# Optimization experiments

Measured on AMD Instinct MI355X. Metric: run time of the kernel, lower is better.

Reference implementation:

```python
import jax, jax.numpy as jnp
import numpy as np

QMIN, QMAX = 0.0, 255.0
# activation statistics (min, max) per layer, from init_kwargs['stats']
STATS = {"conv1": (-0.5, 3.0), "conv2": (0.0, 6.0), "fc1": (0.0, 8.0), "fc2": (0.0, 10.0)}


def calc_scale_zp(min_val, max_val):
    scale = (max_val - min_val) / (QMAX - QMIN)
    # original: int(clamped initial zero point) -> truncation
    zp = jnp.trunc(jnp.clip(QMIN - min_val / scale, QMIN, QMAX))
    return scale, zp


def quantize(x, min_val=None, max_val=None):
    if min_val is None:
        min_val, max_val = x.min(), x.max()
    scale, zp = calc_scale_zp(min_val, max_val)
    q = jnp.round(jnp.clip(zp + x / scale, QMIN, QMAX))
    return q, scale, zp


def conv2d(x, w, b):
    y = jax.lax.conv_general_dilated(x, w, (1, 1), "VALID",
                                     dimension_numbers=("NCHW", "OIHW", "NCHW"))
    return y + b[None, :, None, None]


def linear(x, w, b):
    return x @ w.T + b


def max_pool_2x2(x):
    return jax.lax.reduce_window(x, -jnp.inf, jax.lax.max, (1, 1, 2, 2), (1, 1, 2, 2), "VALID")


def quantize_layer(q_x, scale_x, zp_x, W, B, apply_fn, stat):
    # fake-quant weights/bias with their own min/max
    wq, scale_w, zp_w = quantize(W)
    bq, scale_b, zp_b = quantize(B)
    scale_next, zp_next = calc_scale_zp(stat[0], stat[1])
    X = q_x - zp_x
    W_eff = scale_x * scale_w * (wq - zp_w)
    B_eff = scale_b * (bq + zp_b)  # '+ zp_b' is faithful to the source
    y = jax.nn.relu(apply_fn(X, W_eff, B_eff) / scale_next + zp_next)
    # .round().byte() in torch wraps mod 256
    return jnp.mod(jnp.round(y), 256.0), scale_next, zp_next


def setup_inputs() -> dict:
    key = jax.random.key(0)
    ks = jax.random.split(key, 9)
    B = 4096
    return {
        "x": jax.random.normal(ks[0], (B, 1, 28, 28), jnp.float32),
        "conv1_w": jax.random.normal(ks[1], (20, 1, 5, 5), jnp.float32) * 0.1,
        "conv1_b": jax.random.normal(ks[2], (20,), jnp.float32) * 0.1,
        "conv2_w": jax.random.normal(ks[3], (50, 20, 5, 5), jnp.float32) * 0.05,
        "conv2_b": jax.random.normal(ks[4], (50,), jnp.float32) * 0.05,
        "fc1_w": jax.random.normal(ks[5], (500, 800), jnp.float32) * 0.03,
        "fc1_b": jax.random.normal(ks[6], (500,), jnp.float32) * 0.03,
        "fc2_w": jax.random.normal(ks[7], (10, 500), jnp.float32) * 0.05,
        "fc2_b": jax.random.normal(ks[8], (10,), jnp.float32) * 0.05,
    }


def reference(x, conv1_w, conv1_b, conv2_w, conv2_b, fc1_w, fc1_b, fc2_w, fc2_b):
    q, s, zp = quantize(x, STATS["conv1"][0], STATS["conv1"][1])
    q, s, zp = quantize_layer(q, s, zp, conv1_w, conv1_b, conv2d, STATS["conv2"])
    q = max_pool_2x2(q)                       # [B,20,12,12]
    q, s, zp = quantize_layer(q, s, zp, conv2_w, conv2_b, conv2d, STATS["fc1"])
    q = max_pool_2x2(q)                       # [B,50,4,4]
    q = q.reshape(-1, 4 * 4 * 50)             # [B,800]
    q, s, zp = quantize_layer(q, s, zp, fc1_w, fc1_b, linear, STATS["fc2"])
    xf = s * (q - zp)                         # dequantize
    logits = linear(xf, fc2_w, fc2_b)         # [B,10]
    return jax.nn.log_softmax(logits, axis=1)
```

## Files before the change

### kernel.cpp

```cpp
#include <hip/hip_runtime.h>
#include <cmath>

#define TPB 256
typedef float floatx4 __attribute__((ext_vector_type(4)));
typedef __bf16 bf16x8 __attribute__((ext_vector_type(8)));
typedef unsigned short ushort8 __attribute__((ext_vector_type(8)));
typedef unsigned int uint2v __attribute__((ext_vector_type(2)));
typedef unsigned short ushort_t;

#define OFF_PMN 16
#define OFF_PMX 96
#define OFF_B1 520
#define OFF_B2 544
#define OFF_B3 600
#define W1BF_BYTE 6144
#define W2BF_BYTE 8192
#define W3BF_BYTE 131072
#define PART_BYTE 1048576
#define Q2_BYTE  29360128ULL

#define S_X1 (3.5f/255.0f)
#define ZP_X1 36.0f
#define S_N1 (6.0f/255.0f)
#define S_N2 (8.0f/255.0f)
#define S_N3 (10.0f/255.0f)

#define XSTR 40
#define NCG 4

__device__ inline float qclip(float x, float s, float zp){
    return rintf(fminf(fmaxf(zp + x / s, 0.0f), 255.0f));
}
__device__ inline ushort_t bfbits(float v){
    return (ushort_t)(__float_as_uint(v) >> 16);
}

__global__ __launch_bounds__(TPB) void k_minmax(
        const float* c1w, const float* c1b, const float* c2w, const float* c2b,
        const float* f1w, const float* f1b, float* pmn, float* pmx){
    __shared__ float smn[TPB], smx[TPB];
    int bb = blockIdx.x, tid = threadIdx.x;
    const float* src; int n, sub, nsub;
    if      (bb == 0){ src=c1w; n=500;    sub=0;     nsub=1;  }
    else if (bb == 1){ src=c1b; n=20;     sub=0;     nsub=1;  }
    else if (bb <  6){ src=c2w; n=25000;  sub=bb-2;  nsub=4;  }
    else if (bb == 6){ src=c2b; n=50;     sub=0;     nsub=1;  }
    else if (bb < 71){ src=f1w; n=400000; sub=bb-7;  nsub=64; }
    else             { src=f1b; n=500;    sub=0;     nsub=1;  }
    float mn = INFINITY, mx = -INFINITY;
    for (int i = sub*TPB + tid; i < n; i += nsub*TPB){
        float v = src[i]; mn = fminf(mn, v); mx = fmaxf(mx, v);
    }
    smn[tid] = mn; smx[tid] = mx; __syncthreads();
    for (int s = TPB/2; s > 0; s >>= 1){
        if (tid < s){
            smn[tid] = fminf(smn[tid], smn[tid+s]);
            smx[tid] = fmaxf(smx[tid], smx[tid+s]);
        }
        __syncthreads();
    }
    if (tid == 0){ pmn[bb] = smn[0]; pmx[bb] = smx[0]; }
}

#define N_EFF 452157
__global__ __launch_bounds__(TPB) void k_make_eff(
        const float* c1w, const float* c1b, const float* c2w, const float* c2b,
        const float* f1w, const float* f1b, const float* pmn, const float* pmx,
        float* ws, ushort_t* w1bf, ushort_t* w2bf, ushort_t* w3bf){
    __shared__ float sS[6], sZ[6];
    int tid = threadIdx.x;
    int wv = tid >> 6, lane = tid & 63;
    const int starts[6] = {0,1,2,6,7,71};
    const int counts[6] = {1,1,4,1,64,1};
    #pragma unroll
    for (int rep = 0; rep < 2; ++rep){
        int t = wv + rep*4;
        if (t < 6){
            float mn = INFINITY, mx = -INFINITY;
            if (lane < counts[t]){ mn = pmn[starts[t]+lane]; mx = pmx[starts[t]+lane]; }
            #pragma unroll
            for (int off = 32; off > 0; off >>= 1){
                mn = fminf(mn, __shfl_xor(mn, off));
                mx = fmaxf(mx, __shfl_xor(mx, off));
            }
            if (lane == 0){
                float s = (mx - mn) / 255.0f;
                sS[t] = s;
                sZ[t] = truncf(fminf(fmaxf(0.0f - mn / s, 0.0f), 255.0f));
            }
        }
    }
    __syncthreads();

    int i = blockIdx.x * TPB + tid;
    if (i >= N_EFF) return;
    if (i < 1024){
        int n = i >> 5, k = i & 31;
        float v = 0.0f;
        if (n < 20 && k < 25) v = qclip(c1w[n*25 + k], sS[0], sZ[0]) - sZ[0];
        w1bf[i] = bfbits(v);
    } else if (i < 1044){
        int j = i - 1024;
        ws[OFF_B1 + j] = (sS[1] * (qclip(c1b[j], sS[1], sZ[1]) + sZ[1])) / S_N1;
    } else if (i < 42004){
        int j = i - 1044;
        int c = j >> 11, r = j & 2047, co = r >> 5, k = r & 31;
        int q = k >> 3, jj = k & 7;
        int tap, ci; bool valid;
        if (c < 13){ tap = 2*c + (q>>1); ci = (q&1)*8 + jj; valid = (tap < 25); }
        else       { tap = 4*(c-13) + q; ci = 16 + jj;      valid = (tap < 25) && (jj < 4); }
        valid = valid && (co < 50);
        float v = 0.0f;
        if (valid) v = qclip(c2w[(co*20 + ci)*25 + tap], sS[2], sZ[2]) - sZ[2];
        w2bf[j] = bfbits(v);
    } else if (i < 42054){
        int j = i - 42004;
        ws[OFF_B2 + j] = (sS[3] * (qclip(c2b[j], sS[3], sZ[3]) + sZ[3])) / S_N2;
    } else if (i < 451654){
        int j = i - 42054;
        int n = j / 800, k = j - 800*n;
        float v = 0.0f;
        if (n < 500) v = qclip(f1w[n*800 + k], sS[4], sZ[4]) - sZ[4];
        w3bf[j] = bfbits(v);
    } else if (i < 452154){
        int j = i - 451654;
        ws[OFF_B3 + j] = (sS[5] * (qclip(f1b[j], sS[5], sZ[5]) + sZ[5])) / S_N3;
    } else if (i == 452154){
        ws[0] = (S_N1 * sS[2]) / S_N2;
    } else if (i == 452155){
        ws[1] = (S_N2 * sS[4]) / S_N3;
    } else {
        ws[2] = (S_X1 * sS[0]) / S_N1;
    }
}

__global__ __launch_bounds__(TPB, 4) void k_conv12(const float* x, const ushort_t* w1bf,
                                                   const ushort_t* w2bt, const float* ws,
                                                   ushort_t* q2bf, int B){
    __shared__ __align__(16) ushort_t xs[144*XSTR];
    __shared__ __align__(16) ushort_t xim[3136];
    int b = blockIdx.x, tid = threadIdx.x;
    int lane = tid & 63, wv = tid >> 6;
    int ln = lane & 15, quad = lane >> 4;

    for (int i = tid; i < 144; i += TPB){
        *(unsigned int*)(xs + i*XSTR + 20) = 0u;
        *(unsigned int*)(xs + i*XSTR + 22) = 0u;
    }

    const float* xb = x + (size_t)b * 784;
    if (tid < 196){
        floatx4 v = *(const floatx4*)(xb + tid*4);
        unsigned int qp[2];
        #pragma unroll
        for (int h = 0; h < 2; ++h){
            float q0 = rintf(fminf(fmaxf(ZP_X1 + v[2*h]   / S_X1, 0.0f), 255.0f)) - ZP_X1;
            float q1 = rintf(fminf(fmaxf(ZP_X1 + v[2*h+1] / S_X1, 0.0f), 255.0f)) - ZP_X1;
            qp[h] = (unsigned int)bfbits(q0) | ((unsigned int)bfbits(q1) << 16);
        }
        uint2v qq; qq.x = qp[0]; qq.y = qp[1];
        uint2v* dst = (uint2v*)xim;
        dst[tid]       = qq;
        dst[196 + tid] = qq;
        dst[392 + tid] = qq;
        dst[588 + tid] = qq;
    }

    int offj[8];
    #pragma unroll
    for (int j = 0; j < 8; ++j){
        int k = quad*8 + j;
        int kh = k / 5, kw = k - 5*kh;
        offj[j] = (k < 25) ? (kh*28 + kw) : 0;
    }
    const ushort_t* xq = xim + quad*784;

    ushort8 bw0 = *(const ushort8*)(w1bf + ln*32 + quad*8);
    ushort8 bw1 = *(const ushort8*)(w1bf + (16 + ln)*32 + quad*8);
    bf16x8 bf0 = __builtin_bit_cast(bf16x8, bw0);
    bf16x8 bf1 = __builtin_bit_cast(bf16x8, bw1);

    float K1 = ws[2];
    float B1_0 = ws[OFF_B1 + ln];
    float B1_1 = (ln < 4) ? ws[OFF_B1 + 16 + ln] : 0.0f;
    __syncthreads();

    #pragma unroll 3
    for (int i = 0; i < 9; ++i){
        int mt = 9*wv + i;
        int m = mt*16 + ln;
        int p = m >> 2, crn = m & 3;
        int ph_ = p / 12, pw_ = p - 12*ph_;
        int oh = 2*ph_ + (crn >> 1), ow = 2*pw_ + (crn & 1);
        int base = oh*28 + ow;
        ushort8 aw;
        #pragma unroll
        for (int j = 0; j < 8; ++j)
            aw[j] = xq[base + offj[j]];
        bf16x8 af = __builtin_bit_cast(bf16x8, aw);
        floatx4 z = (floatx4){0.f,0.f,0.f,0.f};
        floatx4 a0 = __builtin_amdgcn_mfma_f32_16x16x32_bf16(af, bf0, z, 0, 0, 0);
        floatx4 a1 = __builtin_amdgcn_mfma_f32_16x16x32_bf16(af, bf1, z, 0, 0, 0);

        int pp = mt*4 + quad;
        {
            float y0 = fmaf(a0[0], K1, B1_0), y1 = fmaf(a0[1], K1, B1_0);
            float y2 = fmaf(a0[2], K1, B1_0), y3 = fmaf(a0[3], K1, B1_0);
            float mA = fmaxf(fmaxf(y0, y1), y2);
            float mf = fmaxf(fmaxf(mA, y3), 0.0f);
            if (__ballot(mf >= 255.5f)){
                unsigned int q0 = ((unsigned int)rintf(fmaxf(y0,0.f))) & 255u;
                unsigned int q1 = ((unsigned int)rintf(fmaxf(y1,0.f))) & 255u;
                unsigned int qq2 = ((unsigned int)rintf(fmaxf(y2,0.f))) & 255u;
                unsigned int q3 = ((unsigned int)rintf(fmaxf(y3,0.f))) & 255u;
                unsigned int h0 = q0 > q1 ? q0 : q1;
                unsigned int h1 = qq2 > q3 ? qq2 : q3;
                mf = (float)(h0 > h1 ? h0 : h1);
            } else {
                mf = rintf(mf);
            }
            xs[pp*XSTR + ln] = bfbits(mf);
        }
        if (ln < 4){
            float y0 = fmaf(a1[0], K1, B1_1), y1 = fmaf(a1[1], K1, B1_1);
            float y2 = fmaf(a1[2], K1, B1_1), y3 = fmaf(a1[3], K1, B1_1);
            float mA = fmaxf(fmaxf(y0, y1), y2);
            float mf = fmaxf(fmaxf(mA, y3), 0.0f);
            if (__ballot(mf >= 255.5f)){
                unsigned int q0 = ((unsigned int)rintf(fmaxf(y0,0.f))) & 255u;
                unsigned int q1 = ((unsigned int)rintf(fmaxf(y1,0.f))) & 255u;
                unsigned int qq2 = ((unsigned int)rintf(fmaxf(y2,0.f))) & 255u;
                unsigned int q3 = ((unsigned int)rintf(fmaxf(y3,0.f))) & 255u;
                unsigned int h0 = q0 > q1 ? q0 : q1;
                unsigned int h1 = qq2 > q3 ? qq2 : q3;
                mf = (float)(h0 > h1 ? h0 : h1);
            } else {
                mf = rintf(mf);
            }
            xs[pp*XSTR + 16 + ln] = bfbits(mf);
        }
    }
    __syncthreads();

    int mt0 = (wv & 1) * 2;
    int nt0 = (wv >> 1) * 2;
    int abase[2];
    #pragma unroll
    for (int mi = 0; mi < 2; ++mi)
        abase[mi] = (24*(mt0+mi) + (ln>>3)*12 + (ln&7)) * XSTR;
    int aoff[20];
    #pragma unroll
    for (int c = 0; c < 20; ++c){
        int tap, inner;
        if (c < 13){ tap = 2*c + (quad>>1); inner = (quad&1)*8; }
        else       { tap = 4*(c-13) + quad; inner = 16; }
        int pt = 0;
        if (tap < 25){ int kh = tap/5, kw = tap-5*kh; pt = kh*12 + kw; }
        aoff[c] = pt*XSTR + inner;
    }

    float sc2d = ws[0];
    const ushort_t* bsrc0 = w2bt + (size_t)(nt0*16 + ln)*32 + quad*8;
    const ushort_t* bsrc1 = bsrc0 + 16*32;

    floatx4 acc[2][2];
    #pragma unroll
    for (int mi = 0; mi < 2; ++mi)
        #pragma unroll
        for (int ni = 0; ni < 2; ++ni) acc[mi][ni] = (floatx4){0.f,0.f,0.f,0.f};

    #pragma unroll
    for (int c = 0; c < 20; ++c){
        ushort8 b0w = *(const ushort8*)(bsrc0 + c*2048);
        ushort8 b1w = *(const ushort8*)(bsrc1 + c*2048);
        ushort8 a0w = *(const ushort8*)(xs + abase[0] + aoff[c]);
        ushort8 a1w = *(const ushort8*)(xs + abase[1] + aoff[c]);
        bf16x8 a0 = __builtin_bit_cast(bf16x8, a0w);
        bf16x8 a1 = __builtin_bit_cast(bf16x8, a1w);
        bf16x8 b0 = __builtin_bit_cast(bf16x8, b0w);
        bf16x8 b1 = __builtin_bit_cast(bf16x8, b1w);
        acc[0][0] = __builtin_amdgcn_mfma_f32_16x16x32_bf16(a0, b0, acc[0][0], 0, 0, 0);
        acc[0][1] = __builtin_amdgcn_mfma_f32_16x16x32_bf16(a0, b1, acc[0][1], 0, 0, 0);
        acc[1][0] = __builtin_amdgcn_mfma_f32_16x16x32_bf16(a1, b0, acc[1][0], 0, 0, 0);
        acc[1][1] = __builtin_amdgcn_mfma_f32_16x16x32_bf16(a1, b1, acc[1][1], 0, 0, 0);
    }

    #pragma unroll
    for (int ni = 0; ni < 2; ++ni){
        int co = (nt0 + ni)*16 + ln;
        float bias2d = (co < 50) ? ws[OFF_B2 + co] : 0.0f;
        #pragma unroll
        for (int mi = 0; mi < 2; ++mi){
            int mt = mt0 + mi;
            float y0 = fmaf(acc[mi][ni][0], sc2d, bias2d);
            float y1 = fmaf(acc[mi][ni][1], sc2d, bias2d);
            float y2 = fmaf(acc[mi][ni][2], sc2d, bias2d);
            float y3 = fmaf(acc[mi][ni][3], sc2d, bias2d);
            float f0 = fmaxf(fmaxf(y0, y1), 0.0f);
            float f1 = fmaxf(fmaxf(y2, y3), 0.0f);
            float g0 = __shfl_xor(f0, 32);
            float g1 = __shfl_xor(f1, 32);
            float v0f = fmaxf(f0, g0), v1f = fmaxf(f1, g1);
            if (__ballot(fmaxf(v0f, v1f) >= 255.5f)){
                unsigned int q0 = ((unsigned int)rintf(fmaxf(y0,0.f))) & 255u;
                unsigned int q1 = ((unsigned int)rintf(fmaxf(y1,0.f))) & 255u;
                unsigned int qq2 = ((unsigned int)rintf(fmaxf(y2,0.f))) & 255u;
                unsigned int q3 = ((unsigned int)rintf(fmaxf(y3,0.f))) & 255u;
                unsigned int h0 = q0 > q1 ? q0 : q1;
                unsigned int h1 = qq2 > q3 ? qq2 : q3;
                unsigned int p0 = (unsigned int)__shfl_xor((int)h0, 32);
                unsigned int p1 = (unsigned int)__shfl_xor((int)h1, 32);
                v0f = (float)(h0 > p0 ? h0 : p0);
                v1f = (float)(h1 > p1 ? h1 : p1);
            } else {
                v0f = rintf(v0f); v1f = rintf(v1f);
            }
            if (quad < 2 && co < 50){
                size_t base = (size_t)b*800 + co*16 + mt*4 + quad*2;
                q2bf[base]     = bfbits(v0f);
                q2bf[base + 1] = bfbits(v1f);
            }
        }
    }
}

__global__ __launch_bounds__(256) void k_fc12(const ushort_t* q2bf, const ushort_t* w3bf,
                                              const float* ws, const float* w2,
                                              float* part, int B){
    __shared__ float red[4*16*10];
    int tid = threadIdx.x;
    int lane = tid & 63, wv = tid >> 6;
    int ln = lane & 15, quad = lane >> 4;
    int bi = blockIdx.x;
    int cg = bi & (NCG-1);
    int b0 = (bi >> 2) * 16;
    int n0 = cg*128 + wv*32;

    const ushort_t* asrc = q2bf + (size_t)(b0 + ln)*800 + quad*8;
    const ushort_t* bsrc = w3bf + (size_t)(n0 + ln)*800 + quad*8;

    floatx4 acc[2];
    acc[0] = (floatx4){0.f,0.f,0.f,0.f};
    acc[1] = (floatx4){0.f,0.f,0.f,0.f};

    for (int c = 0; c < 25; ++c){
        ushort8 aw = *(const ushort8*)(asrc + c*32);
        bf16x8 af = __builtin_bit_cast(bf16x8, aw);
        ushort8 b0w = *(const ushort8*)(bsrc + c*32);
        ushort8 b1w = *(const ushort8*)(bsrc + 16*800 + c*32);
        acc[0] = __builtin_amdgcn_mfma_f32_16x16x32_bf16(
                     af, __builtin_bit_cast(bf16x8, b0w), acc[0], 0, 0, 0);
        acc[1] = __builtin_amdgcn_mfma_f32_16x16x32_bf16(
                     af, __builtin_bit_cast(bf16x8, b1w), acc[1], 0, 0, 0);
    }

    float sc3d = ws[1];
    float xf[4][2];
    #pragma unroll
    for (int t = 0; t < 2; ++t){
        int col = n0 + t*16 + ln;
        float bias = (col < 500) ? ws[OFF_B3 + col] : 0.0f;
        #pragma unroll
        for (int r = 0; r < 4; ++r){
            float y = fmaxf(fmaf(acc[t][r], sc3d, bias), 0.0f);
            unsigned int q = ((unsigned int)rintf(y)) & 255u;
            xf[r][t] = (col < 500) ? S_N3 * (float)q : 0.0f;
        }
    }

    #pragma unroll
    for (int c = 0; c < 10; ++c){
        float p[4] = {0.f, 0.f, 0.f, 0.f};
        #pragma unroll
        for (int t = 0; t < 2; ++t){
            int col = n0 + t*16 + ln;
            float w = (col < 500) ? w2[c*500 + col] : 0.0f;
            #pragma unroll
            for (int r = 0; r < 4; ++r) p[r] = fmaf(xf[r][t], w, p[r]);
        }
        #pragma unroll
        for (int m = 1; m <= 8; m <<= 1)
            #pragma unroll
            for (int r = 0; r < 4; ++r) p[r] += __shfl_xor(p[r], m);
        if (ln == 0){
            #pragma unroll
            for (int r = 0; r < 4; ++r)
                red[(wv*16 + quad*4 + r)*10 + c] = p[r];
        }
    }
    __syncthreads();

    if (tid < 160){
        int row = tid / 10, c = tid - 10*(tid/10);
        float s = red[row*10 + c] + red[160 + row*10 + c]
                + red[320 + row*10 + c] + red[480 + row*10 + c];
        part[((size_t)cg*B + b0 + row)*10 + c] = s;
    }
}

__global__ __launch_bounds__(256) void k_softmax(const float* part, const float* b2,
                                                 float* out, int B){
    int i = blockIdx.x*256 + threadIdx.x;
    if (i >= B) return;
    float lg[10], mx = -INFINITY;
    #pragma unroll
    for (int c = 0; c < 10; ++c){
        float s = b2[c];
        #pragma unroll
        for (int g = 0; g < NCG; ++g) s += part[((size_t)g*B + i)*10 + c];
        lg[c] = s; mx = fmaxf(mx, s);
    }
    float sum = 0.0f;
    #pragma unroll
    for (int c = 0; c < 10; ++c) sum += expf(lg[c] - mx);
    float ls = logf(sum);
    #pragma unroll
    for (int c = 0; c < 10; ++c)
        out[(size_t)i*10 + c] = lg[c] - mx - ls;
}

extern "C" void kernel_launch(void* const* d_in, const int* in_sizes, int n_in,
                              void* d_out, int out_size, void* d_ws, size_t ws_size,
                              hipStream_t stream){
    const float* x   = (const float*)d_in[0];
    const float* c1w = (const float*)d_in[1];
    const float* c1b = (const float*)d_in[2];
    const float* c2w = (const float*)d_in[3];
    const float* c2b = (const float*)d_in[4];
    const float* f1w = (const float*)d_in[5];
    const float* f1b = (const float*)d_in[6];
    const float* f2w = (const float*)d_in[7];
    const float* f2b = (const float*)d_in[8];
    int B = in_sizes[0] / 784;

    float* ws = (float*)d_ws;
    float* pmn = ws + OFF_PMN;
    float* pmx = ws + OFF_PMX;
    ushort_t* w1bf = (ushort_t*)((char*)d_ws + W1BF_BYTE);
    ushort_t* w2bf = (ushort_t*)((char*)d_ws + W2BF_BYTE);
    ushort_t* w3bf = (ushort_t*)((char*)d_ws + W3BF_BYTE);
    float* part = (float*)((char*)d_ws + PART_BYTE);
    ushort_t* q2bf = (ushort_t*)((char*)d_ws + Q2_BYTE);
    float* out = (float*)d_out;

    k_minmax<<<72, TPB, 0, stream>>>(c1w, c1b, c2w, c2b, f1w, f1b, pmn, pmx);
    k_make_eff<<<(N_EFF + TPB - 1)/TPB, TPB, 0, stream>>>(c1w, c1b, c2w, c2b, f1w, f1b, pmn, pmx, ws, w1bf, w2bf, w3bf);
    k_conv12<<<B, TPB, 0, stream>>>(x, w1bf, w2bf, ws, q2bf, B);
    k_fc12<<<(B/16)*NCG, 256, 0, stream>>>(q2bf, w3bf, ws, f2w, part, B);
    k_softmax<<<(B + 255)/256, 256, 0, stream>>>(part, f2b, out, B);
}
```

Measured before the change: 159.2 us.

## Fuse softmax into fc kernel via last-block atomic ticket; prefetch fc loads

Removes the separate log-softmax launch. Each 16-row group of fc blocks increments an atomic ticket counter, and the last of the four column-group blocks sums the partial logits and writes the log-softmax output. The counters are reset at the start of the conv kernel. The fc inner loop is also fully unrolled with software prefetch of the next A and B fragments. The cost is extra fences and atomics, plus reliance on the conv kernel clearing the tick array; that clearing only covers 256 counters while B/16 is 256.

```diff
diff --git a/kernel.cpp b/kernel.cpp
--- a/kernel.cpp
+++ b/kernel.cpp
@@ -10,6 +10,7 @@
 
 #define OFF_PMN 16
 #define OFF_PMX 96
+#define OFF_TICK 256
 #define OFF_B1 520
 #define OFF_B2 544
 #define OFF_B3 600
@@ -136,12 +137,14 @@
 
 __global__ __launch_bounds__(TPB, 4) void k_conv12(const float* x, const ushort_t* w1bf,
                                                    const ushort_t* w2bt, const float* ws,
-                                                   ushort_t* q2bf, int B){
+                                                   ushort_t* q2bf, int* tick, int B){
     __shared__ __align__(16) ushort_t xs[144*XSTR];
     __shared__ __align__(16) ushort_t xim[3136];
     int b = blockIdx.x, tid = threadIdx.x;
     int lane = tid & 63, wv = tid >> 6;
     int ln = lane & 15, quad = lane >> 4;
+
+    if (tid == 0 && b < 256) tick[b] = 0;
 
     for (int i = tid; i < 144; i += TPB){
         *(unsigned int*)(xs + i*XSTR + 20) = 0u;
@@ -326,32 +329,45 @@
 
 __global__ __launch_bounds__(256) void k_fc12(const ushort_t* q2bf, const ushort_t* w3bf,
                                               const float* ws, const float* w2,
-                                              float* part, int B){
+                                              const float* b2, float* part, float* out,
+                                              int* tick, int B){
     __shared__ float red[4*16*10];
+    __shared__ int sLast;
     int tid = threadIdx.x;
     int lane = tid & 63, wv = tid >> 6;
     int ln = lane & 15, quad = lane >> 4;
     int bi = blockIdx.x;
     int cg = bi & (NCG-1);
-    int b0 = (bi >> 2) * 16;
+    int gi = bi >> 2;
+    int b0 = gi * 16;
     int n0 = cg*128 + wv*32;
 
     const ushort_t* asrc = q2bf + (size_t)(b0 + ln)*800 + quad*8;
-    const ushort_t* bsrc = w3bf + (size_t)(n0 + ln)*800 + quad*8;
+    const ushort_t* bsrc0 = w3bf + (size_t)(n0 + ln)*800 + quad*8;
+    const ushort_t* bsrc1 = bsrc0 + 16*800;
 
     floatx4 acc[2];
     acc[0] = (floatx4){0.f,0.f,0.f,0.f};
     acc[1] = (floatx4){0.f,0.f,0.f,0.f};
 
+    ushort8 aw  = *(const ushort8*)(asrc);
+    ushort8 b0w = *(const ushort8*)(bsrc0);
+    ushort8 b1w = *(const ushort8*)(bsrc1);
+    #pragma unroll
     for (int c = 0; c < 25; ++c){
-        ushort8 aw = *(const ushort8*)(asrc + c*32);
-        bf16x8 af = __builtin_bit_cast(bf16x8, aw);
-        ushort8 b0w = *(const ushort8*)(bsrc + c*32);
-        ushort8 b1w = *(const ushort8*)(bsrc + 16*800 + c*32);
+        ushort8 aN, b0N, b1N;
+        if (c < 24){
+            aN  = *(const ushort8*)(asrc  + (c+1)*32);
+            b0N = *(const ushort8*)(bsrc0 + (c+1)*32);
+            b1N = *(const ushort8*)(bsrc1 + (c+1)*32);
+        }
         acc[0] = __builtin_amdgcn_mfma_f32_16x16x32_bf16(
-                     af, __builtin_bit_cast(bf16x8, b0w), acc[0], 0, 0, 0);
+                     __builtin_bit_cast(bf16x8, aw), __builtin_bit_cast(bf16x8, b0w),
+                     acc[0], 0, 0, 0);
         acc[1] = __builtin_amdgcn_mfma_f32_16x16x32_bf16(
-                     af, __builtin_bit_cast(bf16x8, b1w), acc[1], 0, 0, 0);
+                     __builtin_bit_cast(bf16x8, aw), __builtin_bit_cast(bf16x8, b1w),
+                     acc[1], 0, 0, 0);
+        aw = aN; b0w = b0N; b1w = b1N;
     }
 
     float sc3d = ws[1];
@@ -396,27 +412,36 @@
                 + red[320 + row*10 + c] + red[480 + row*10 + c];
         part[((size_t)cg*B + b0 + row)*10 + c] = s;
     }
-}
-
-__global__ __launch_bounds__(256) void k_softmax(const float* part, const float* b2,
-                                                 float* out, int B){
-    int i = blockIdx.x*256 + threadIdx.x;
-    if (i >= B) return;
-    float lg[10], mx = -INFINITY;
-    #pragma unroll
-    for (int c = 0; c < 10; ++c){
-        float s = b2[c];
-        #pragma unroll
-        for (int g = 0; g < NCG; ++g) s += part[((size_t)g*B + i)*10 + c];
-        lg[c] = s; mx = fmaxf(mx, s);
-    }
-    float sum = 0.0f;
-    #pragma unroll
-    for (int c = 0; c < 10; ++c) sum += expf(lg[c] - mx);
-    float ls = logf(sum);
-    #pragma unroll
-    for (int c = 0; c < 10; ++c)
-        out[(size_t)i*10 + c] = lg[c] - mx - ls;
+
+    __syncthreads();
+    if (tid == 0){
+        __threadfence();
+        int old = atomicAdd(&tick[gi], 1);
+        sLast = (old == NCG - 1);
+    }
+    __syncthreads();
+    if (sLast){
+        __threadfence();
+        if (tid < 16){
+            int row = b0 + tid;
+            const volatile float* pv = part;
+            float lg[10], mx = -INFINITY;
+            #pragma unroll
+            for (int c = 0; c < 10; ++c){
+                float s = b2[c];
+                #pragma unroll
+                for (int g = 0; g < NCG; ++g) s += pv[((size_t)g*B + row)*10 + c];
+                lg[c] = s; mx = fmaxf(mx, s);
+            }
+            float sum = 0.0f;
+            #pragma unroll
+            for (int c = 0; c < 10; ++c) sum += expf(lg[c] - mx);
+            float ls = logf(sum);
+            #pragma unroll
+            for (int c = 0; c < 10; ++c)
+                out[(size_t)row*10 + c] = lg[c] - mx - ls;
+        }
+    }
 }
 
 extern "C" void kernel_launch(void* const* d_in, const int* in_sizes, int n_in,
@@ -436,6 +461,7 @@
     float* ws = (float*)d_ws;
     float* pmn = ws + OFF_PMN;
     float* pmx = ws + OFF_PMX;
+    int* tick = (int*)(ws + OFF_TICK);
     ushort_t* w1bf = (ushort_t*)((char*)d_ws + W1BF_BYTE);
     ushort_t* w2bf = (ushort_t*)((char*)d_ws + W2BF_BYTE);
     ushort_t* w3bf = (ushort_t*)((char*)d_ws + W3BF_BYTE);
@@ -445,7 +471,6 @@
 
     k_minmax<<<72, TPB, 0, stream>>>(c1w, c1b, c2w, c2b, f1w, f1b, pmn, pmx);
     k_make_eff<<<(N_EFF + TPB - 1)/TPB, TPB, 0, stream>>>(c1w, c1b, c2w, c2b, f1w, f1b, pmn, pmx, ws, w1bf, w2bf, w3bf);
-    k_conv12<<<B, TPB, 0, stream>>>(x, w1bf, w2bf, ws, q2bf, B);
-    k_fc12<<<(B/16)*NCG, 256, 0, stream>>>(q2bf, w3bf, ws, f2w, part, B);
-    k_softmax<<<(B + 255)/256, 256, 0, stream>>>(part, f2b, out, B);
-}
+    k_conv12<<<B, TPB, 0, stream>>>(x, w1bf, w2bf, ws, q2bf, tick, B);
+    k_fc12<<<(B/16)*NCG, 256, 0, stream>>>(q2bf, w3bf, ws, f2w, f2b, part, out, tick, B);
+}
```

Result: slower. 233.1 us (+46.4%).

## Tile fc operands into MFMA-friendly blocks and fuse log-softmax into fc kernel

Applied to the files above, without the earlier changes.

Rewrites the fc1 weights and the conv2 output into 16x32 tiled layouts, so each MFMA fragment load reads a contiguous 1 KB block instead of striding 800 elements. The fc kernel now uses 512 threads per 16-row batch group covering all 512 output columns, with software-prefetched register double buffering. It computes log-softmax in-block, which removes the partial-sum buffer and the separate softmax launch. The trade-off is fewer blocks (B/16) with heavier per-block work and a small serial tail on 16 threads.

```diff
diff --git a/kernel.cpp b/kernel.cpp
--- a/kernel.cpp
+++ b/kernel.cpp
@@ -16,7 +16,6 @@
 #define W1BF_BYTE 6144
 #define W2BF_BYTE 8192
 #define W3BF_BYTE 131072
-#define PART_BYTE 1048576
 #define Q2_BYTE  29360128ULL
 
 #define S_X1 (3.5f/255.0f)
@@ -26,7 +25,6 @@
 #define S_N3 (10.0f/255.0f)
 
 #define XSTR 40
-#define NCG 4
 
 __device__ inline float qclip(float x, float s, float zp){
     return rintf(fminf(fmaxf(zp + x / s, 0.0f), 255.0f));
@@ -121,7 +119,7 @@
         int n = j / 800, k = j - 800*n;
         float v = 0.0f;
         if (n < 500) v = qclip(f1w[n*800 + k], sS[4], sZ[4]) - sZ[4];
-        w3bf[j] = bfbits(v);
+        w3bf[(((n>>4)*25 + (k>>5))*16 + (n&15))*32 + (k&31)] = bfbits(v);
     } else if (i < 452154){
         int j = i - 451654;
         ws[OFF_B3 + j] = (sS[5] * (qclip(f1b[j], sS[5], sZ[5]) + sZ[5])) / S_N3;
@@ -285,6 +283,7 @@
         acc[1][1] = __builtin_amdgcn_mfma_f32_16x16x32_bf16(a1, b1, acc[1][1], 0, 0, 0);
     }
 
+    int bg = b >> 4, brow = b & 15;
     #pragma unroll
     for (int ni = 0; ni < 2; ++ni){
         int co = (nt0 + ni)*16 + ln;
@@ -316,49 +315,61 @@
                 v0f = rintf(v0f); v1f = rintf(v1f);
             }
             if (quad < 2 && co < 50){
-                size_t base = (size_t)b*800 + co*16 + mt*4 + quad*2;
-                q2bf[base]     = bfbits(v0f);
-                q2bf[base + 1] = bfbits(v1f);
-            }
-        }
-    }
-}
-
-__global__ __launch_bounds__(256) void k_fc12(const ushort_t* q2bf, const ushort_t* w3bf,
+                int k0 = co*16 + mt*4 + quad*2;
+                size_t off = ((size_t)bg*25 + (k0 >> 5))*512 + brow*32 + (k0 & 31);
+                q2bf[off]     = bfbits(v0f);
+                q2bf[off + 1] = bfbits(v1f);
+            }
+        }
+    }
+}
+
+__global__ __launch_bounds__(512) void k_fc12(const ushort_t* q2t, const ushort_t* w3t,
                                               const float* ws, const float* w2,
-                                              float* part, int B){
-    __shared__ float red[4*16*10];
+                                              const float* b2, float* out, int B){
+    __shared__ float red[8*16*10];
     int tid = threadIdx.x;
     int lane = tid & 63, wv = tid >> 6;
     int ln = lane & 15, quad = lane >> 4;
-    int bi = blockIdx.x;
-    int cg = bi & (NCG-1);
-    int b0 = (bi >> 2) * 16;
-    int n0 = cg*128 + wv*32;
-
-    const ushort_t* asrc = q2bf + (size_t)(b0 + ln)*800 + quad*8;
-    const ushort_t* bsrc = w3bf + (size_t)(n0 + ln)*800 + quad*8;
-
-    floatx4 acc[2];
-    acc[0] = (floatx4){0.f,0.f,0.f,0.f};
-    acc[1] = (floatx4){0.f,0.f,0.f,0.f};
-
+    int gi = blockIdx.x;
+    int b0 = gi * 16;
+
+    const ushort_t* asrc = q2t + (size_t)gi*25*512 + ln*32 + quad*8;
+    const ushort_t* bsrc = w3t + (size_t)(wv*4)*25*512 + ln*32 + quad*8;
+
+    floatx4 acc[4];
+    #pragma unroll
+    for (int t = 0; t < 4; ++t) acc[t] = (floatx4){0.f,0.f,0.f,0.f};
+
+    ushort8 aw = *(const ushort8*)(asrc);
+    ushort8 bw[4];
+    #pragma unroll
+    for (int t = 0; t < 4; ++t) bw[t] = *(const ushort8*)(bsrc + t*12800);
+
+    #pragma unroll
     for (int c = 0; c < 25; ++c){
-        ushort8 aw = *(const ushort8*)(asrc + c*32);
-        bf16x8 af = __builtin_bit_cast(bf16x8, aw);
-        ushort8 b0w = *(const ushort8*)(bsrc + c*32);
-        ushort8 b1w = *(const ushort8*)(bsrc + 16*800 + c*32);
-        acc[0] = __builtin_amdgcn_mfma_f32_16x16x32_bf16(
-                     af, __builtin_bit_cast(bf16x8, b0w), acc[0], 0, 0, 0);
-        acc[1] = __builtin_amdgcn_mfma_f32_16x16x32_bf16(
-                     af, __builtin_bit_cast(bf16x8, b1w), acc[1], 0, 0, 0);
+        ushort8 aN; ushort8 bN[4];
+        if (c < 24){
+            aN = *(const ushort8*)(asrc + (c+1)*512);
+            #pragma unroll
+            for (int t = 0; t < 4; ++t)
+                bN[t] = *(const ushort8*)(bsrc + t*12800 + (c+1)*512);
+        }
+        #pragma unroll
+        for (int t = 0; t < 4; ++t)
+            acc[t] = __builtin_amdgcn_mfma_f32_16x16x32_bf16(
+                         __builtin_bit_cast(bf16x8, aw), __builtin_bit_cast(bf16x8, bw[t]),
+                         acc[t], 0, 0, 0);
+        aw = aN;
+        #pragma unroll
+        for (int t = 0; t < 4; ++t) bw[t] = bN[t];
     }
 
     float sc3d = ws[1];
-    float xf[4][2];
-    #pragma unroll
-    for (int t = 0; t < 2; ++t){
-        int col = n0 + t*16 + ln;
+    float xf[4][4];
+    #pragma unroll
+    for (int t = 0; t < 4; ++t){
+        int col = wv*64 + t*16 + ln;
         float bias = (col < 500) ? ws[OFF_B3 + col] : 0.0f;
         #pragma unroll
         for (int r = 0; r < 4; ++r){
@@ -372,8 +383,8 @@
     for (int c = 0; c < 10; ++c){
         float p[4] = {0.f, 0.f, 0.f, 0.f};
         #pragma unroll
-        for (int t = 0; t < 2; ++t){
-            int col = n0 + t*16 + ln;
+        for (int t = 0; t < 4; ++t){
+            int col = wv*64 + t*16 + ln;
             float w = (col < 500) ? w2[c*500 + col] : 0.0f;
             #pragma unroll
             for (int r = 0; r < 4; ++r) p[r] = fmaf(xf[r][t], w, p[r]);
@@ -390,33 +401,24 @@
     }
     __syncthreads();
 
-    if (tid < 160){
-        int row = tid / 10, c = tid - 10*(tid/10);
-        float s = red[row*10 + c] + red[160 + row*10 + c]
-                + red[320 + row*10 + c] + red[480 + row*10 + c];
-        part[((size_t)cg*B + b0 + row)*10 + c] = s;
-    }
-}
-
-__global__ __launch_bounds__(256) void k_softmax(const float* part, const float* b2,
-                                                 float* out, int B){
-    int i = blockIdx.x*256 + threadIdx.x;
-    if (i >= B) return;
-    float lg[10], mx = -INFINITY;
-    #pragma unroll
-    for (int c = 0; c < 10; ++c){
-        float s = b2[c];
-        #pragma unroll
-        for (int g = 0; g < NCG; ++g) s += part[((size_t)g*B + i)*10 + c];
-        lg[c] = s; mx = fmaxf(mx, s);
-    }
-    float sum = 0.0f;
-    #pragma unroll
-    for (int c = 0; c < 10; ++c) sum += expf(lg[c] - mx);
-    float ls = logf(sum);
-    #pragma unroll
-    for (int c = 0; c < 10; ++c)
-        out[(size_t)i*10 + c] = lg[c] - mx - ls;
+    if (tid < 16){
+        int row = tid;
+        float lg[10], mx = -INFINITY;
+        #pragma unroll
+        for (int c = 0; c < 10; ++c){
+            float s = b2[c];
+            #pragma unroll
+            for (int w = 0; w < 8; ++w) s += red[(w*16 + row)*10 + c];
+            lg[c] = s; mx = fmaxf(mx, s);
+        }
+        float sum = 0.0f;
+        #pragma unroll
+        for (int c = 0; c < 10; ++c) sum += expf(lg[c] - mx);
+        float ls = logf(sum);
+        #pragma unroll
+        for (int c = 0; c < 10; ++c)
+            out[(size_t)(b0 + row)*10 + c] = lg[c] - mx - ls;
+    }
 }
 
 extern "C" void kernel_launch(void* const* d_in, const int* in_sizes, int n_in,
@@ -439,13 +441,11 @@
     ushort_t* w1bf = (ushort_t*)((char*)d_ws + W1BF_BYTE);
     ushort_t* w2bf = (ushort_t*)((char*)d_ws + W2BF_BYTE);
     ushort_t* w3bf = (ushort_t*)((char*)d_ws + W3BF_BYTE);
-    float* part = (float*)((char*)d_ws + PART_BYTE);
     ushort_t* q2bf = (ushort_t*)((char*)d_ws + Q2_BYTE);
     float* out = (float*)d_out;
 
     k_minmax<<<72, TPB, 0, stream>>>(c1w, c1b, c2w, c2b, f1w, f1b, pmn, pmx);
     k_make_eff<<<(N_EFF + TPB - 1)/TPB, TPB, 0, stream>>>(c1w, c1b, c2w, c2b, f1w, f1b, pmn, pmx, ws, w1bf, w2bf, w3bf);
     k_conv12<<<B, TPB, 0, stream>>>(x, w1bf, w2bf, ws, q2bf, B);
-    k_fc12<<<(B/16)*NCG, 256, 0, stream>>>(q2bf, w3bf, ws, f2w, part, B);
-    k_softmax<<<(B + 255)/256, 256, 0, stream>>>(part, f2b, out, B);
-}
+    k_fc12<<<B/16, 512, 0, stream>>>(q2bf, w3bf, ws, f2w, f2b, out, B);
+}
```

Result: faster. 154.3 us (-3.1%).
